# Performance work log

Hardware: AMD Instinct MI355X
Metric: run time of the kernel (lower is better)

## Reference

```python
import jax, jax.numpy as jnp
import numpy as np

N = 8192      # nodes
F = 256       # input feature dim
D_OUT = 256   # output_dim


def setup_inputs() -> dict:
    key = jax.random.key(0)
    k1, k2, k3 = jax.random.split(key, 3)
    data = jax.random.normal(k1, (1, N, F), dtype=jnp.float32)
    # dense (normalized) adjacency; the original converts dense->sparse then matmuls,
    # which is mathematically a dense adj @ data product.
    adj = jax.random.uniform(k2, (1, N, N), dtype=jnp.float32)
    kernel = jax.random.normal(k3, (F, D_OUT), dtype=jnp.float32)
    return {"data": data, "adj": adj, "kernel": kernel}


def reference(data, adj, kernel):
    # af = adj @ data  : [N, N] @ [N, F] -> [N, F]  (neighbor aggregation)
    af = jnp.matmul(adj[0], data[0])
    # dense projection: [N, F] @ [F, D_OUT] -> [N, D_OUT]
    out = jnp.matmul(af, kernel)
    # expand batch dim back and apply activation (relu)
    return jax.nn.relu(out[None, :, :])
```

## Files before the change

kernel.cpp:

```cpp
#include <hip/hip_runtime.h>
#include <stdint.h>

#define AS1 __attribute__((address_space(1)))
#define AS3 __attribute__((address_space(3)))

typedef float f32x4 __attribute__((ext_vector_type(4)));
typedef __bf16 bf16x8 __attribute__((ext_vector_type(8)));
typedef uint32_t u32x2 __attribute__((ext_vector_type(2)));
typedef unsigned short u16;
typedef u16 u16x8 __attribute__((ext_vector_type(8)));

__device__ __forceinline__ unsigned short f2bf(float f) {
    uint32_t x = __float_as_uint(f);
    x += 0x7FFFu + ((x >> 16) & 1u);
    return (unsigned short)(x >> 16);
}
__device__ __forceinline__ float bf2f(unsigned short u) {
    return __uint_as_float((uint32_t)u << 16);
}

__device__ __forceinline__ void gload_lds16(const void* g, void* l) {
    __builtin_amdgcn_global_load_lds((const AS1 void*)g, (AS3 void*)l, 16, 0, 0);
}

__global__ __launch_bounds__(256) void wt_kernel(const float* __restrict__ W,
                                                 unsigned short* __restrict__ WT) {
    __shared__ float tile[32][33];
    const int bf = blockIdx.x & 7;
    const int bn = blockIdx.x >> 3;
    const int t = threadIdx.x;
    const int c = t & 31, r = t >> 5;
#pragma unroll
    for (int i = 0; i < 4; ++i)
        tile[r + i * 8][c] = W[(bf * 32 + r + i * 8) * 256 + bn * 32 + c];
    __syncthreads();
#pragma unroll
    for (int i = 0; i < 4; ++i)
        WT[(bn * 32 + r + i * 8) * 256 + bf * 32 + c] = f2bf(tile[c][r + i * 8]);
}

template <int LDA, int LDB, int KSTEPS>
__global__ __launch_bounds__(256) void gemm1_kernel(const float* __restrict__ A,
                                                    const unsigned short* __restrict__ B,
                                                    unsigned short* __restrict__ dkT) {
    __shared__ unsigned short Alds[32 * 64];
    __shared__ unsigned short Blds[256 * 64];

    const int t = threadIdx.x;
    const int w = t >> 6;
    const int l = t & 63;
    const int m0 = blockIdx.x * 32;

    const int ar = t >> 3;
    const int kq = t & 7;
    const float* gA = A + (size_t)(m0 + ar) * LDA + kq * 4;
    char* aw0 = (char*)Alds + ((ar * 128 + kq * 8) ^ ((ar & 7) << 4));
    char* aw1 = (char*)Alds + ((ar * 128 + 64 + kq * 8) ^ ((ar & 7) << 4));

    const int nr_base = w * 64 + (l >> 3);
    const int c16 = l & 7;

    f32x4 acc[2][4];
#pragma unroll
    for (int i = 0; i < 2; ++i)
#pragma unroll
        for (int j = 0; j < 4; ++j) acc[i][j] = (f32x4){0.f, 0.f, 0.f, 0.f};

    for (int step = 0; step < KSTEPS; ++step) {
        const int k0 = step * 64;
        __syncthreads();
#pragma unroll
        for (int i = 0; i < 8; ++i) {
            const int nr = nr_base + i * 8;
            const unsigned short* src =
                B + (size_t)nr * LDB + k0 + ((c16 ^ (nr & 7)) << 3);
            gload_lds16(src, (char*)Blds + (w * 512 + i * 64) * 16);
        }
        const f32x4 v0 = *(const f32x4*)(gA + k0);
        const f32x4 v1 = *(const f32x4*)(gA + k0 + 32);
        uint32_t p0 = (uint32_t)f2bf(v0.x) | ((uint32_t)f2bf(v0.y) << 16);
        uint32_t p1 = (uint32_t)f2bf(v0.z) | ((uint32_t)f2bf(v0.w) << 16);
        uint32_t p2 = (uint32_t)f2bf(v1.x) | ((uint32_t)f2bf(v1.y) << 16);
        uint32_t p3 = (uint32_t)f2bf(v1.z) | ((uint32_t)f2bf(v1.w) << 16);
        ((uint32_t*)aw0)[0] = p0;
        ((uint32_t*)aw0)[1] = p1;
        ((uint32_t*)aw1)[0] = p2;
        ((uint32_t*)aw1)[1] = p3;
        __syncthreads();
#pragma unroll
        for (int kh = 0; kh < 2; ++kh) {
            const int koffb = kh * 64 + ((l >> 4) << 4);
            bf16x8 af[2], bv[4];
#pragma unroll
            for (int im = 0; im < 2; ++im) {
                const int r = im * 16 + (l & 15);
                af[im] = *(const bf16x8*)((const char*)Alds +
                                          ((r * 128 + koffb) ^ ((r & 7) << 4)));
            }
#pragma unroll
            for (int jn = 0; jn < 4; ++jn) {
                const int n = w * 64 + jn * 16 + (l & 15);
                bv[jn] = *(const bf16x8*)((const char*)Blds +
                                          ((n * 128 + koffb) ^ ((n & 7) << 4)));
            }
#pragma unroll
            for (int im = 0; im < 2; ++im)
#pragma unroll
                for (int jn = 0; jn < 4; ++jn)
                    acc[im][jn] = __builtin_amdgcn_mfma_f32_16x16x32_bf16(
                        af[im], bv[jn], acc[im][jn], 0, 0, 0);
        }
    }

    __syncthreads();
    u16* T = (u16*)Blds;
#pragma unroll
    for (int im = 0; im < 2; ++im) {
        const int mq = im * 16 + ((l >> 4) << 2);
#pragma unroll
        for (int jn = 0; jn < 4; ++jn) {
            const int n = w * 64 + jn * 16 + (l & 15);
            u32x2 pk;
            pk[0] = (uint32_t)f2bf(acc[im][jn][0]) |
                    ((uint32_t)f2bf(acc[im][jn][1]) << 16);
            pk[1] = (uint32_t)f2bf(acc[im][jn][2]) |
                    ((uint32_t)f2bf(acc[im][jn][3]) << 16);
            *(u32x2*)((char*)T + n * 80 + mq * 2) = pk;
        }
    }
    __syncthreads();
    {
        const int n = t;
        const char* src = (const char*)T + n * 80;
        char* dst = (char*)(dkT + (size_t)n * 8192 + m0);
#pragma unroll
        for (int i = 0; i < 4; ++i)
            *(f32x4*)(dst + i * 16) = *(const f32x4*)(src + i * 16);
    }
}

template <int KSPLIT>
__global__ __launch_bounds__(256, 3) void gemm2_kernel(const float* __restrict__ A,
                                                       const unsigned short* __restrict__ B,
                                                       float* __restrict__ Out0,
                                                       u16* __restrict__ Pws) {
    __shared__ unsigned short Alds[64 * 64];
    __shared__ unsigned short Blds[256 * 64];

    const int t = threadIdx.x;
    const int w = t >> 6;
    const int l = t & 63;
    const int mtile = blockIdx.x / KSPLIT;
    const int ks = blockIdx.x % KSPLIT;
    const int m0 = mtile * 64;
    const int kbase = ks * (8192 / KSPLIT);
    constexpr int KSTEPS = (8192 / KSPLIT) / 64;

    const int jr = t >> 4;
    const int jc = t & 15;
    const float* gA = A + (size_t)(m0 + jr) * 8192 + kbase + jc * 4;

    const int nr_base = w * 64 + (l >> 3);
    const int c16 = l & 7;

    f32x4 acc[4][4];
#pragma unroll
    for (int i = 0; i < 4; ++i)
#pragma unroll
        for (int j = 0; j < 4; ++j) acc[i][j] = (f32x4){0.f, 0.f, 0.f, 0.f};

    const int q = l >> 4;
    const int li = l & 15;

    for (int step = 0; step < KSTEPS; ++step) {
        const int k0 = step * 64;
        __syncthreads();
#pragma unroll
        for (int i = 0; i < 8; ++i) {
            const int nr = nr_base + i * 8;
            const unsigned short* src =
                B + (size_t)nr * 8192 + kbase + k0 + ((c16 ^ (nr & 7)) << 3);
            gload_lds16(src, (char*)Blds + (w * 512 + i * 64) * 16);
        }
#pragma unroll
        for (int j = 0; j < 4; ++j) {
            const f32x4 v = __builtin_nontemporal_load(
                (const f32x4*)(gA + (size_t)j * 16 * 8192 + k0));
            const int r = j * 16 + jr;
            const int p = (jc >> 1) ^ (r & 7);
            u32x2 pk;
            pk[0] = (uint32_t)f2bf(v.x) | ((uint32_t)f2bf(v.y) << 16);
            pk[1] = (uint32_t)f2bf(v.z) | ((uint32_t)f2bf(v.w) << 16);
            *(u32x2*)((char*)Alds + r * 128 + p * 16 + (jc & 1) * 8) = pk;
        }
        __syncthreads();
#pragma unroll
        for (int kh = 0; kh < 2; ++kh) {
            const int koffb = kh * 64 + (q << 4);
            bf16x8 af[4], bv[4];
#pragma unroll
            for (int im = 0; im < 4; ++im) {
                const int r = im * 16 + li;
                af[im] = *(const bf16x8*)((const char*)Alds +
                                          ((r * 128 + koffb) ^ ((r & 7) << 4)));
            }
#pragma unroll
            for (int jn = 0; jn < 4; ++jn) {
                const int n = w * 64 + jn * 16 + li;
                bv[jn] = *(const bf16x8*)((const char*)Blds +
                                          ((n * 128 + koffb) ^ ((n & 7) << 4)));
            }
#pragma unroll
            for (int im = 0; im < 4; ++im)
#pragma unroll
                for (int jn = 0; jn < 4; ++jn)
                    acc[im][jn] = __builtin_amdgcn_mfma_f32_16x16x32_bf16(
                        af[im], bv[jn], acc[im][jn], 0, 0, 0);
        }
    }

    if (KSPLIT == 1) {
#pragma unroll
        for (int im = 0; im < 4; ++im) {
            const int row0 = m0 + im * 16 + (q << 2);
#pragma unroll
            for (int jn = 0; jn < 4; ++jn) {
                const int col = w * 64 + jn * 16 + li;
#pragma unroll
                for (int r = 0; r < 4; ++r) {
                    const float v = acc[im][jn][r];
                    Out0[(size_t)(row0 + r) * 256 + col] = v > 0.f ? v : 0.f;
                }
            }
        }
    } else {
        u16* Pb = Pws + (size_t)ks * (8192 * 256);
#pragma unroll
        for (int im = 0; im < 4; ++im) {
            const int row0 = m0 + im * 16 + (q << 2);
#pragma unroll
            for (int jn = 0; jn < 4; ++jn) {
                const int col = w * 64 + jn * 16 + li;
#pragma unroll
                for (int r = 0; r < 4; ++r)
                    Pb[(size_t)(row0 + r) * 256 + col] = f2bf(acc[im][jn][r]);
            }
        }
    }
}

template <int S>
__global__ __launch_bounds__(256) void reduce_relu_kernel(float* __restrict__ out,
                                                          const u16* __restrict__ P) {
    const size_t i = (size_t)blockIdx.x * 256 + threadIdx.x;
    float s0 = 0, s1 = 0, s2 = 0, s3 = 0, s4 = 0, s5 = 0, s6 = 0, s7 = 0;
#pragma unroll
    for (int s = 0; s < S; ++s) {
        const u16x8 v = ((const u16x8*)(P + (size_t)s * (8192 * 256)))[i];
        s0 += bf2f(v[0]); s1 += bf2f(v[1]); s2 += bf2f(v[2]); s3 += bf2f(v[3]);
        s4 += bf2f(v[4]); s5 += bf2f(v[5]); s6 += bf2f(v[6]); s7 += bf2f(v[7]);
    }
    f32x4 lo, hi;
    lo.x = s0 > 0.f ? s0 : 0.f; lo.y = s1 > 0.f ? s1 : 0.f;
    lo.z = s2 > 0.f ? s2 : 0.f; lo.w = s3 > 0.f ? s3 : 0.f;
    hi.x = s4 > 0.f ? s4 : 0.f; hi.y = s5 > 0.f ? s5 : 0.f;
    hi.z = s6 > 0.f ? s6 : 0.f; hi.w = s7 > 0.f ? s7 : 0.f;
    ((f32x4*)out)[2 * i] = lo;
    ((f32x4*)out)[2 * i + 1] = hi;
}

extern "C" void kernel_launch(void* const* d_in, const int* in_sizes, int n_in,
                              void* d_out, int out_size, void* d_ws, size_t ws_size,
                              hipStream_t stream) {
    const float* data = (const float*)d_in[0];
    const float* adj = (const float*)d_in[1];
    const float* Wk = (const float*)d_in[2];
    float* out = (float*)d_out;

    unsigned short* WT = (unsigned short*)d_ws;
    unsigned short* dkT = (unsigned short*)((char*)d_ws + 131072);
    u16* Pb = (u16*)((char*)d_ws + 131072 + 4194304);

    const size_t base_need = 131072 + 4194304;
    const size_t part_bytes = (size_t)8192 * 256 * 2;

    wt_kernel<<<64, 256, 0, stream>>>(Wk, WT);
    gemm1_kernel<256, 256, 4><<<256, 256, 0, stream>>>(data, WT, dkT);
    if (ws_size >= base_need + 8 * part_bytes) {
        gemm2_kernel<8><<<1024, 256, 0, stream>>>(adj, dkT, out, Pb);
        reduce_relu_kernel<8><<<1024, 256, 0, stream>>>(out, Pb);
    } else if (ws_size >= base_need + 2 * part_bytes) {
        gemm2_kernel<2><<<256, 256, 0, stream>>>(adj, dkT, out, Pb);
        reduce_relu_kernel<2><<<1024, 256, 0, stream>>>(out, Pb);
    } else {
        gemm2_kernel<1><<<128, 256, 0, stream>>>(adj, dkT, out, nullptr);
    }
}
```

Baseline: 103.7 us.

## Enlarge gemm2 M tile to 128 rows and raise split-K to sixteen

The adjacency GEMM block now covers 128 rows instead of 64. Each wave owns 32 rows across all 256 columns, so every B tile loaded into LDS is reused across twice as many A rows, halving B traffic per output. Split-K rises from 8 to 16 to keep 1024 blocks. That doubles the bf16 partial-sum workspace and the reduction reads, and 128 accumulators per thread increase register pressure. The A loads also drop the nontemporal hint.

```diff
diff --git a/kernel.cpp b/kernel.cpp
--- a/kernel.cpp
+++ b/kernel.cpp
@@ -144,33 +144,34 @@
                                                        const unsigned short* __restrict__ B,
                                                        float* __restrict__ Out0,
                                                        u16* __restrict__ Pws) {
-    __shared__ unsigned short Alds[64 * 64];
+    __shared__ unsigned short Alds[128 * 64];
     __shared__ unsigned short Blds[256 * 64];
 
     const int t = threadIdx.x;
     const int w = t >> 6;
     const int l = t & 63;
+    const int q = l >> 4;
+    const int li = l & 15;
     const int mtile = blockIdx.x / KSPLIT;
     const int ks = blockIdx.x % KSPLIT;
-    const int m0 = mtile * 64;
+    const int m0 = mtile * 128;
     const int kbase = ks * (8192 / KSPLIT);
     constexpr int KSTEPS = (8192 / KSPLIT) / 64;
 
     const int jr = t >> 4;
     const int jc = t & 15;
     const float* gA = A + (size_t)(m0 + jr) * 8192 + kbase + jc * 4;
+    const int ap = (jc >> 1) ^ (jr & 7);
+    char* const awbase = (char*)Alds + jr * 128 + ap * 16 + (jc & 1) * 8;
 
     const int nr_base = w * 64 + (l >> 3);
     const int c16 = l & 7;
 
-    f32x4 acc[4][4];
-#pragma unroll
-    for (int i = 0; i < 4; ++i)
-#pragma unroll
-        for (int j = 0; j < 4; ++j) acc[i][j] = (f32x4){0.f, 0.f, 0.f, 0.f};
-
-    const int q = l >> 4;
-    const int li = l & 15;
+    f32x4 acc[2][16];
+#pragma unroll
+    for (int i = 0; i < 2; ++i)
+#pragma unroll
+        for (int j = 0; j < 16; ++j) acc[i][j] = (f32x4){0.f, 0.f, 0.f, 0.f};
 
     for (int step = 0; step < KSTEPS; ++step) {
         const int k0 = step * 64;
@@ -183,49 +184,44 @@
             gload_lds16(src, (char*)Blds + (w * 512 + i * 64) * 16);
         }
 #pragma unroll
-        for (int j = 0; j < 4; ++j) {
-            const f32x4 v = __builtin_nontemporal_load(
-                (const f32x4*)(gA + (size_t)j * 16 * 8192 + k0));
-            const int r = j * 16 + jr;
-            const int p = (jc >> 1) ^ (r & 7);
+        for (int j = 0; j < 8; ++j) {
+            const f32x4 v = *(const f32x4*)(gA + (size_t)j * 16 * 8192 + k0);
             u32x2 pk;
             pk[0] = (uint32_t)f2bf(v.x) | ((uint32_t)f2bf(v.y) << 16);
             pk[1] = (uint32_t)f2bf(v.z) | ((uint32_t)f2bf(v.w) << 16);
-            *(u32x2*)((char*)Alds + r * 128 + p * 16 + (jc & 1) * 8) = pk;
+            *(u32x2*)(awbase + j * 16 * 128) = pk;
         }
         __syncthreads();
 #pragma unroll
         for (int kh = 0; kh < 2; ++kh) {
             const int koffb = kh * 64 + (q << 4);
-            bf16x8 af[4], bv[4];
-#pragma unroll
-            for (int im = 0; im < 4; ++im) {
-                const int r = im * 16 + li;
+            bf16x8 af[2];
+#pragma unroll
+            for (int im = 0; im < 2; ++im) {
+                const int r = w * 32 + im * 16 + li;
                 af[im] = *(const bf16x8*)((const char*)Alds +
                                           ((r * 128 + koffb) ^ ((r & 7) << 4)));
             }
 #pragma unroll
-            for (int jn = 0; jn < 4; ++jn) {
-                const int n = w * 64 + jn * 16 + li;
-                bv[jn] = *(const bf16x8*)((const char*)Blds +
-                                          ((n * 128 + koffb) ^ ((n & 7) << 4)));
-            }
-#pragma unroll
-            for (int im = 0; im < 4; ++im)
-#pragma unroll
-                for (int jn = 0; jn < 4; ++jn)
-                    acc[im][jn] = __builtin_amdgcn_mfma_f32_16x16x32_bf16(
-                        af[im], bv[jn], acc[im][jn], 0, 0, 0);
+            for (int jn = 0; jn < 16; ++jn) {
+                const int n = jn * 16 + li;
+                const bf16x8 bv = *(const bf16x8*)((const char*)Blds +
+                                                   ((n * 128 + koffb) ^ ((n & 7) << 4)));
+                acc[0][jn] = __builtin_amdgcn_mfma_f32_16x16x32_bf16(
+                    af[0], bv, acc[0][jn], 0, 0, 0);
+                acc[1][jn] = __builtin_amdgcn_mfma_f32_16x16x32_bf16(
+                    af[1], bv, acc[1][jn], 0, 0, 0);
+            }
         }
     }
 
     if (KSPLIT == 1) {
 #pragma unroll
-        for (int im = 0; im < 4; ++im) {
-            const int row0 = m0 + im * 16 + (q << 2);
-#pragma unroll
-            for (int jn = 0; jn < 4; ++jn) {
-                const int col = w * 64 + jn * 16 + li;
+        for (int im = 0; im < 2; ++im) {
+            const int row0 = m0 + w * 32 + im * 16 + (q << 2);
+#pragma unroll
+            for (int jn = 0; jn < 16; ++jn) {
+                const int col = jn * 16 + li;
 #pragma unroll
                 for (int r = 0; r < 4; ++r) {
                     const float v = acc[im][jn][r];
@@ -236,11 +232,11 @@
     } else {
         u16* Pb = Pws + (size_t)ks * (8192 * 256);
 #pragma unroll
-        for (int im = 0; im < 4; ++im) {
-            const int row0 = m0 + im * 16 + (q << 2);
-#pragma unroll
-            for (int jn = 0; jn < 4; ++jn) {
-                const int col = w * 64 + jn * 16 + li;
+        for (int im = 0; im < 2; ++im) {
+            const int row0 = m0 + w * 32 + im * 16 + (q << 2);
+#pragma unroll
+            for (int jn = 0; jn < 16; ++jn) {
+                const int col = jn * 16 + li;
 #pragma unroll
                 for (int r = 0; r < 4; ++r)
                     Pb[(size_t)(row0 + r) * 256 + col] = f2bf(acc[im][jn][r]);
@@ -286,13 +282,13 @@
 
     wt_kernel<<<64, 256, 0, stream>>>(Wk, WT);
     gemm1_kernel<256, 256, 4><<<256, 256, 0, stream>>>(data, WT, dkT);
-    if (ws_size >= base_need + 8 * part_bytes) {
-        gemm2_kernel<8><<<1024, 256, 0, stream>>>(adj, dkT, out, Pb);
-        reduce_relu_kernel<8><<<1024, 256, 0, stream>>>(out, Pb);
+    if (ws_size >= base_need + 16 * part_bytes) {
+        gemm2_kernel<16><<<1024, 256, 0, stream>>>(adj, dkT, out, Pb);
+        reduce_relu_kernel<16><<<1024, 256, 0, stream>>>(out, Pb);
     } else if (ws_size >= base_need + 2 * part_bytes) {
-        gemm2_kernel<2><<<256, 256, 0, stream>>>(adj, dkT, out, Pb);
+        gemm2_kernel<2><<<128, 256, 0, stream>>>(adj, dkT, out, Pb);
         reduce_relu_kernel<2><<<1024, 256, 0, stream>>>(out, Pb);
     } else {
-        gemm2_kernel<1><<<128, 256, 0, stream>>>(adj, dkT, out, nullptr);
-    }
-}
+        gemm2_kernel<1><<<64, 256, 0, stream>>>(adj, dkT, out, nullptr);
+    }
+}
```

Result: slower. 203.5 us (+96.3%).
